# Optimization experiments

Hardware: AMD Instinct MI355X
Metric: run time of the kernel (lower is better)

The kernel has to match this reference:

```python
import jax, jax.numpy as jnp
import numpy as np

T, B, E, H, L = 512, 64, 300, 800, 3  # seq, batch, embed, per-layer hidden, layers


def setup_inputs() -> dict:
    key = jax.random.key(0)
    ks = jax.random.split(key, 8)
    s = 0.05
    return {
        "sent": jax.random.normal(ks[0], (T, B, E), jnp.float32),
        "lengths": jax.random.randint(ks[1], (B,), 1, T + 1),
        "W0": jax.random.normal(ks[2], (E, 3 * H), jnp.float32) * s,
        "b0": jnp.zeros((3 * H,), jnp.float32),
        "W1": jax.random.normal(ks[3], (H, 3 * H), jnp.float32) * s,
        "b1": jnp.zeros((3 * H,), jnp.float32),
        "W2": jax.random.normal(ks[4], (H, 3 * H), jnp.float32) * s,
        "b2": jnp.zeros((3 * H,), jnp.float32),
    }


def _fo_pool(f, z):
    # c_t = f_t * z_t + (1 - f_t) * c_{t-1}, c_0 = 0  (ForgetMult)
    # linear recurrence c_t = a_t * c_{t-1} + b_t with a = 1-f, b = f*z
    a = 1.0 - f
    b = f * z
    def comb(c1, c2):
        a1, b1 = c1
        a2, b2 = c2
        return (a2 * a1, a2 * b1 + b2)
    _, C = jax.lax.associative_scan(comb, (a, b), axis=0)
    return C  # [T,B,H]; initial state is zero so C is exactly the pooled state


def _qrnn_layer(x, W, b):
    g = jnp.einsum('tbe,eh->tbh', x, W) + b  # [T,B,3H]
    z, f, o = jnp.split(g, 3, axis=-1)
    C = _fo_pool(jax.nn.sigmoid(f), jnp.tanh(z))
    return jax.nn.sigmoid(o) * C, C[-1]


def reference(sent, lengths, W0, b0, W1, b1, W2, b2):
    h = sent
    finals = []
    for W, bb in ((W0, b0), (W1, b1), (W2, b2)):
        h, c_last = _qrnn_layer(h, W, bb)
        finals.append(c_last)
    hn = jnp.stack(finals, axis=0)            # [L,B,H]
    out = jnp.transpose(hn, (1, 0, 2)).reshape(B, L * H)  # [B, L*H]
    return out
```

## Files before the change

### kernel.cpp

```cpp
#include <hip/hip_runtime.h>
#include <hip/hip_bf16.h>
#include <cstdint>
#include <cstddef>


typedef __bf16 bf16_t;
typedef __bf16 bf16x8 __attribute__((ext_vector_type(8)));
typedef float f32x4 __attribute__((ext_vector_type(4)));

#define T_C 128
#define NCHUNK 4
#define BATCH 64
#define EMB 300
#define HID 800
#define LDH 832
#define MC (T_C * BATCH)
#define CAST_OPS (MC * 320 / 8)

__device__ __forceinline__ float fast_sigmoid(float x) {
  return 1.0f / (1.0f + __expf(-x));
}
__device__ __forceinline__ float fast_tanh(float x) {
  return 2.0f / (1.0f + __expf(-2.0f * x)) - 1.0f;
}
__device__ __forceinline__ float b2f(uint32_t u) {
  union { uint32_t i; float f; } x;
  x.i = u << 16;
  return x.f;
}

__device__ __forceinline__ void cast_op(const float* __restrict__ X,
                                        bf16_t* __restrict__ Y, int cc,
                                        int id) {
  const int rr = id / 40, cb = id - rr * 40;
  const int b = rr >> 7, t = rr & 127;
  const float* src = X + (size_t)((cc * 128 + t) * 64 + b) * EMB + cb * 8;
  bf16x8 w;
  if (cb < 37) {
    const f32x4 v0 = *(const f32x4*)src;
    const f32x4 v1 = *(const f32x4*)(src + 4);
#pragma unroll
    for (int e = 0; e < 4; ++e) {
      w[e] = (bf16_t)v0[e];
      w[e + 4] = (bf16_t)v1[e];
    }
  } else {
#pragma unroll
    for (int e = 0; e < 8; ++e) {
      const int col = cb * 8 + e;
      w[e] = (bf16_t)((col < EMB) ? src[e] : 0.0f);
    }
  }
  *(bf16x8*)&Y[((size_t)cc * MC + rr) * 320 + cb * 8] = w;
}

__global__ __launch_bounds__(256) void prep_all(
    const float* __restrict__ W0, const float* __restrict__ W1,
    const float* __restrict__ W2, bf16_t* __restrict__ M0,
    bf16_t* __restrict__ M1, bf16_t* __restrict__ Z2,
    const float* __restrict__ sent, bf16_t* __restrict__ A0) {
  const int z = blockIdx.z;
  if (z == 3) {
    const int id = (blockIdx.y * gridDim.x + blockIdx.x) * 256 + threadIdx.x;
    if (id < CAST_OPS) cast_op(sent, A0, 0, id);
    return;
  }
  const float* W = z == 0 ? W0 : (z == 1 ? W1 : W2);
  bf16_t* Wt = z == 0 ? M0 : (z == 1 ? M1 : Z2);
  const int K = z == 0 ? 300 : 800;
  const int Kpad = z == 0 ? 320 : 832;
  const int Npad = (z < 2) ? 2496 : 1664;
  const int i = blockIdx.x, j = blockIdx.y;
  if (i * 32 >= Npad || j * 32 >= Kpad) return;
  __shared__ float tile[32][33];
  const int tx = threadIdx.x & 31, ty = threadIdx.x >> 5;
#pragma unroll
  for (int r = 0; r < 32; r += 8) {
    const int k = j * 32 + ty + r;
    const int n = i * 32 + tx;
    int h, src;
    if (z < 2) {
      const int jt = n / 192, rr = n - jt * 192;
      if (rr < 128) {
        h = jt * 64 + (rr >> 1);
        src = (rr & 1) * 800 + h;
      } else {
        h = jt * 64 + (rr - 128);
        src = 1600 + h;
      }
    } else {
      h = n >> 1;
      src = (n & 1) * 800 + h;
    }
    const bool valid = (k < K) && (h < 800);
    tile[ty + r][tx] = valid ? W[(size_t)k * 2400 + src] : 0.0f;
  }
  __syncthreads();
#pragma unroll
  for (int r = 0; r < 32; r += 8) {
    const int n = i * 32 + ty + r, k = j * 32 + tx;
    if (n < Npad && k < Kpad)
      Wt[(size_t)n * Kpad + k] = (bf16_t)tile[tx][ty + r];
  }
}

__device__ __forceinline__ void stage16(const bf16_t* gp, bf16_t* lp) {
  __builtin_amdgcn_global_load_lds((__attribute__((address_space(1))) void*)gp,
                                   (__attribute__((address_space(3))) void*)lp,
                                   16, 0, 0);
}

template <int NTF, int ETS>
__device__ __forceinline__ void gemm_tile_to_lds(
    const bf16_t* __restrict__ A, const bf16_t* __restrict__ Bt,
    bf16_t* __restrict__ S, int K, int mBase, int nBase) {
  bf16_t* As = S;
  bf16_t* Bs = S + 8192;
  const int tid = threadIdx.x;
  const int wave = tid >> 6, lane = tid & 63;
  const int wm = wave >> 1, wn = wave & 1;
  const int srow = tid >> 3;
  const int scolSw = ((tid & 7) ^ (srow & 7)) * 8;
  const size_t aBase = (size_t)(mBase + srow) * K + scolSw;
  const size_t bBase = (size_t)(nBase + srow) * K + scolSw;
  const int ldsOff = tid * 8;

  f32x4 acc[4][NTF];
#pragma unroll
  for (int mt = 0; mt < 4; ++mt)
#pragma unroll
    for (int nt = 0; nt < NTF; ++nt) {
      f32x4 zz = {0.0f, 0.0f, 0.0f, 0.0f};
      acc[mt][nt] = zz;
    }

  const int fr = lane & 15, fq = lane >> 4;
  const int x0 = fr & 7;
  const int ckEl0 = (fq ^ x0) * 8;
  const int ckEl1 = ((4 + fq) ^ x0) * 8;

  for (int k0 = 0; k0 < K; k0 += 64) {
#pragma unroll
    for (int p = 0; p < 4; ++p)
      stage16(A + aBase + (size_t)(32 * p) * K + k0, &As[ldsOff + p * 2048]);
#pragma unroll
    for (int p = 0; p < NTF; ++p)
      stage16(Bt + bBase + (size_t)(32 * p) * K + k0, &Bs[ldsOff + p * 2048]);
    __syncthreads();
#pragma unroll
    for (int kh = 0; kh < 2; ++kh) {
      const int ck = kh ? ckEl1 : ckEl0;
      bf16x8 af[4], bfv[NTF];
#pragma unroll
      for (int mt = 0; mt < 4; ++mt)
        af[mt] = *(const bf16x8*)&As[(wm * 64 + mt * 16 + fr) * 64 + ck];
#pragma unroll
      for (int nt = 0; nt < NTF; ++nt)
        bfv[nt] = *(const bf16x8*)&Bs[(wn * (16 * NTF) + nt * 16 + fr) * 64 + ck];
#pragma unroll
      for (int mt = 0; mt < 4; ++mt)
#pragma unroll
        for (int nt = 0; nt < NTF; ++nt)
          acc[mt][nt] = __builtin_amdgcn_mfma_f32_16x16x32_bf16(
              af[mt], bfv[nt], acc[mt][nt], 0, 0, 0);
    }
    __syncthreads();
  }
  bf16_t* Et = S;
#pragma unroll
  for (int mt = 0; mt < 4; ++mt)
#pragma unroll
    for (int nt = 0; nt < NTF; ++nt)
#pragma unroll
      for (int r = 0; r < 4; ++r)
        Et[(wm * 64 + mt * 16 + fq * 4 + r) * ETS + wn * (16 * NTF) + nt * 16 +
           fr] = (bf16_t)acc[mt][nt][r];
  __syncthreads();
}

__device__ __forceinline__ void scan_h_body(
    const bf16_t* __restrict__ A, const bf16_t* __restrict__ Wm,
    const float* __restrict__ bias, bf16_t* __restrict__ Hout,
    float* __restrict__ carry, float* __restrict__ outC, int K, int outOff,
    int first, int last, int b, int ntile, bf16_t* S, float (*SA)[64],
    float (*SB)[64], float (*SC)[64]) {
  gemm_tile_to_lds<6, 196>(A, Wm, S, K, b * 128, ntile * 192);

  const uint32_t* Ep = (const uint32_t*)S;
  const int tid = threadIdx.x;
  const int hl = tid & 63, s = tid >> 6;
  const int h = ntile * 64 + hl;
  const bool hOK = (h < HID);
  const int hb = hOK ? h : 0;
  const float bz = bias[hb], bf = bias[hb + 800], bo = bias[hb + 1600];

  float av[32], bv[32];
  float Aa = 1.0f, Bb = 0.0f;
#pragma unroll
  for (int q = 0; q < 32; ++q) {
    const int t = s * 32 + q;
    const uint32_t v = Ep[t * 98 + hl];
    const float zv = fast_tanh(b2f(v & 0xffffu) + bz);
    const float fv = fast_sigmoid(b2f(v >> 16) + bf);
    av[q] = 1.0f - fv;
    bv[q] = fv * zv;
    Aa *= av[q];
    Bb = fmaf(av[q], Bb, bv[q]);
  }
  SA[s][hl] = Aa;
  SB[s][hl] = Bb;
  __syncthreads();
  if (tid < 64) {
    const int h2 = ntile * 64 + tid;
    const bool ok2 = (h2 < HID);
    float c = (first || !ok2) ? 0.0f : carry[b * HID + h2];
#pragma unroll
    for (int ss = 0; ss < 4; ++ss) {
      SC[ss][tid] = c;
      c = fmaf(SA[ss][tid], c, SB[ss][tid]);
    }
    if (ok2) {
      carry[b * HID + h2] = c;
      if (last) outC[b * 2400 + outOff + h2] = c;
    }
  }
  __syncthreads();
  float c = SC[s][hl];
#pragma unroll
  for (int q = 0; q < 32; ++q) {
    const int t = s * 32 + q;
    c = fmaf(av[q], c, bv[q]);
    const float o = fast_sigmoid((float)S[t * 196 + 128 + hl] + bo);
    Hout[(size_t)(b * 128 + t) * LDH + h] =
        hOK ? (bf16_t)(o * c) : (bf16_t)0.0f;
  }
}

__device__ __forceinline__ void scan_c_body(
    const bf16_t* __restrict__ A, const bf16_t* __restrict__ Wzf,
    const float* __restrict__ bias, float* __restrict__ carry,
    float* __restrict__ outC, int K, int outOff, int first, int last, int b,
    int ntile, bf16_t* S, float (*SA)[64], float (*SB)[64]) {
  gemm_tile_to_lds<4, 140>(A, Wzf, S, K, b * 128, ntile * 128);

  const uint32_t* Ep = (const uint32_t*)S;
  const int tid = threadIdx.x;
  const int hl = tid & 63, s = tid >> 6;
  const int h = ntile * 64 + hl;
  const int hb = (h < HID) ? h : 0;
  const float bz = bias[hb], bf = bias[hb + 800];

  float Aa = 1.0f, Bb = 0.0f;
#pragma unroll
  for (int q = 0; q < 32; ++q) {
    const int t = s * 32 + q;
    const uint32_t v = Ep[t * 70 + hl];
    const float zv = fast_tanh(b2f(v & 0xffffu) + bz);
    const float fv = fast_sigmoid(b2f(v >> 16) + bf);
    const float a = 1.0f - fv;
    Aa *= a;
    Bb = fmaf(a, Bb, fv * zv);
  }
  SA[s][hl] = Aa;
  SB[s][hl] = Bb;
  __syncthreads();
  if (tid < 64) {
    const int h2 = ntile * 64 + tid;
    const bool ok2 = (h2 < HID);
    float c = (first || !ok2) ? 0.0f : carry[b * HID + h2];
#pragma unroll
    for (int ss = 0; ss < 4; ++ss) c = fmaf(SA[ss][tid], c, SB[ss][tid]);
    if (ok2) {
      carry[b * HID + h2] = c;
      if (last) outC[b * 2400 + outOff + h2] = c;
    }
  }
}

__device__ __forceinline__ void block_tile(int& b, int& ntile) {
  const int nT = 13;
  const int L = blockIdx.y * nT + blockIdx.x;
  const int xcd = L & 7, j = L >> 3;
  b = xcd * 8 + j / nT;
  ntile = j % nT;
}

struct Role {
  const bf16_t* A;
  const bf16_t* W;
  const float* bias;
  bf16_t* Hout;
  float* carry;
  int K;
  int outOff;
  int type;
  int first;
  int last;
};

__global__ __launch_bounds__(256, 3) void gemm_scan_multi(
    Role r0, Role r1, Role r2, Role r3, float* __restrict__ outC) {
  __shared__ __align__(16) bf16_t S[25088];
  __shared__ float SA[4][64], SB[4][64], SC[4][64];
  const Role r = blockIdx.z == 0
                     ? r0
                     : (blockIdx.z == 1 ? r1 : (blockIdx.z == 2 ? r2 : r3));
  if (r.type == 3) {
    int id = (blockIdx.y * gridDim.x + blockIdx.x) * 256 + threadIdx.x;
    const int stride = gridDim.x * gridDim.y * 256;
#pragma unroll
    for (int it = 0; it < 2; ++it, id += stride)
      if (id < CAST_OPS) cast_op((const float*)r.A, r.Hout, r.outOff, id);
    return;
  }
  int b, ntile;
  block_tile(b, ntile);
  if (r.type == 1)
    scan_h_body(r.A, r.W, r.bias, r.Hout, r.carry, outC, r.K, r.outOff,
                r.first, r.last, b, ntile, S, SA, SB, SC);
  else
    scan_c_body(r.A, r.W, r.bias, r.carry, outC, r.K, r.outOff, r.first,
                r.last, b, ntile, S, SA, SB);
}

extern "C" void kernel_launch(void* const* d_in, const int* in_sizes, int n_in,
                              void* d_out, int out_size, void* d_ws, size_t ws_size,
                              hipStream_t stream) {
  const float* sent = (const float*)d_in[0];
  const float* W0 = (const float*)d_in[2];
  const float* b0 = (const float*)d_in[3];
  const float* W1 = (const float*)d_in[4];
  const float* b1 = (const float*)d_in[5];
  const float* W2 = (const float*)d_in[6];
  const float* b2 = (const float*)d_in[7];
  float* out = (float*)d_out;

  char* ws = (char*)d_ws;
  size_t off = 0;
  auto alloc = [&](size_t bytes) {
    void* p = ws + off;
    off += (bytes + 255) & ~(size_t)255;
    return p;
  };
  bf16_t* Wm0 = (bf16_t*)alloc((size_t)2496 * 320 * 2);
  bf16_t* Wm1 = (bf16_t*)alloc((size_t)2496 * 832 * 2);
  bf16_t* Wzf2 = (bf16_t*)alloc((size_t)1664 * 832 * 2);
  bf16_t* A0 = (bf16_t*)alloc((size_t)32768 * 320 * 2);
  bf16_t* H0buf[2], *H1buf[2];
  H0buf[0] = (bf16_t*)alloc((size_t)MC * LDH * 2);
  H0buf[1] = (bf16_t*)alloc((size_t)MC * LDH * 2);
  H1buf[0] = (bf16_t*)alloc((size_t)MC * LDH * 2);
  H1buf[1] = (bf16_t*)alloc((size_t)MC * LDH * 2);
  float* car0 = (float*)alloc((size_t)BATCH * HID * 4);
  float* car1 = (float*)alloc((size_t)BATCH * HID * 4);
  float* car2 = (float*)alloc((size_t)BATCH * HID * 4);
  if (off > ws_size) return;

  prep_all<<<dim3(78, 26, 4), 256, 0, stream>>>(W0, W1, W2, Wm0, Wm1, Wzf2,
                                                sent, A0);

  auto mkL0 = [&](int c) -> Role {
    return Role{A0 + (size_t)c * MC * 320, Wm0, b0, H0buf[c & 1], car0,
                320, 0, 1, c == 0, c == NCHUNK - 1};
  };
  auto mkL1 = [&](int c) -> Role {
    return Role{H0buf[c & 1], Wm1, b1, H1buf[c & 1], car1,
                832, 800, 1, c == 0, c == NCHUNK - 1};
  };
  auto mkL2 = [&](int c) -> Role {
    return Role{H1buf[c & 1], Wzf2, b2, nullptr, car2,
                832, 1600, 2, c == 0, c == NCHUNK - 1};
  };
  auto mkCast = [&](int c) -> Role {
    return Role{(const bf16_t*)sent, nullptr, nullptr, A0, nullptr,
                0, c, 3, 0, 0};
  };

  {
    Role a = mkL0(0), c1 = mkCast(1), c2 = mkCast(2), c3 = mkCast(3);
    gemm_scan_multi<<<dim3(13, 64, 4), 256, 0, stream>>>(a, c1, c2, c3, out);
  }
  {
    Role a = mkL1(0), b_ = mkL0(1);
    gemm_scan_multi<<<dim3(13, 64, 2), 256, 0, stream>>>(a, b_, b_, b_, out);
  }
  for (int c = 1; c <= 2; ++c) {
    Role a = mkL1(c), b_ = mkL2(c - 1), d = mkL0(c + 1);
    gemm_scan_multi<<<dim3(13, 64, 3), 256, 0, stream>>>(a, b_, d, d, out);
  }
  {
    Role a = mkL1(3), b_ = mkL2(2);
    gemm_scan_multi<<<dim3(13, 64, 2), 256, 0, stream>>>(a, b_, b_, b_, out);
  }
  {
    Role a = mkL2(3);
    gemm_scan_multi<<<dim3(13, 64, 1), 256, 0, stream>>>(a, a, a, a, out);
  }
}
```

Baseline: 465.4 us.

## Fold biases into GEMM via ones column; add dedicated last-chunk layer-2 kernel

Bias vectors are written into the padding row k==K of the transposed weight matrices. A matching constant 1.0 is placed in the first padding column of the activation inputs (the cast input and the hidden outputs at h==800), so the GEMM adds the bias itself and the epilogue no longer loads or adds it. A separate smaller-LDS kernel with launch bounds allowing 4 blocks per CU handles the final layer-2 chunk, replacing the generic multi-role kernel there. The bias is now rounded to bf16, which adds a little error, and the change relies on the padding columns being exactly 1 and 0.

```diff
diff --git a/kernel.cpp b/kernel.cpp
--- a/kernel.cpp
+++ b/kernel.cpp
@@ -48,7 +48,8 @@
 #pragma unroll
     for (int e = 0; e < 8; ++e) {
       const int col = cb * 8 + e;
-      w[e] = (bf16_t)((col < EMB) ? src[e] : 0.0f);
+      float v = (col < EMB) ? src[e] : (col == EMB ? 1.0f : 0.0f);
+      w[e] = (bf16_t)v;
     }
   }
   *(bf16x8*)&Y[((size_t)cc * MC + rr) * 320 + cb * 8] = w;
@@ -56,8 +57,9 @@
 
 __global__ __launch_bounds__(256) void prep_all(
     const float* __restrict__ W0, const float* __restrict__ W1,
-    const float* __restrict__ W2, bf16_t* __restrict__ M0,
-    bf16_t* __restrict__ M1, bf16_t* __restrict__ Z2,
+    const float* __restrict__ W2, const float* __restrict__ B0,
+    const float* __restrict__ B1, const float* __restrict__ B2,
+    bf16_t* __restrict__ M0, bf16_t* __restrict__ M1, bf16_t* __restrict__ Z2,
     const float* __restrict__ sent, bf16_t* __restrict__ A0) {
   const int z = blockIdx.z;
   if (z == 3) {
@@ -66,6 +68,7 @@
     return;
   }
   const float* W = z == 0 ? W0 : (z == 1 ? W1 : W2);
+  const float* Bv = z == 0 ? B0 : (z == 1 ? B1 : B2);
   bf16_t* Wt = z == 0 ? M0 : (z == 1 ? M1 : Z2);
   const int K = z == 0 ? 300 : 800;
   const int Kpad = z == 0 ? 320 : 832;
@@ -92,8 +95,12 @@
       h = n >> 1;
       src = (n & 1) * 800 + h;
     }
-    const bool valid = (k < K) && (h < 800);
-    tile[ty + r][tx] = valid ? W[(size_t)k * 2400 + src] : 0.0f;
+    float v = 0.0f;
+    if (h < 800) {
+      if (k < K) v = W[(size_t)k * 2400 + src];
+      else if (k == K) v = Bv[src];
+    }
+    tile[ty + r][tx] = v;
   }
   __syncthreads();
 #pragma unroll
@@ -180,10 +187,9 @@
 
 __device__ __forceinline__ void scan_h_body(
     const bf16_t* __restrict__ A, const bf16_t* __restrict__ Wm,
-    const float* __restrict__ bias, bf16_t* __restrict__ Hout,
-    float* __restrict__ carry, float* __restrict__ outC, int K, int outOff,
-    int first, int last, int b, int ntile, bf16_t* S, float (*SA)[64],
-    float (*SB)[64], float (*SC)[64]) {
+    bf16_t* __restrict__ Hout, float* __restrict__ carry,
+    float* __restrict__ outC, int K, int outOff, int first, int last, int b,
+    int ntile, bf16_t* S, float (*SA)[64], float (*SB)[64], float (*SC)[64]) {
   gemm_tile_to_lds<6, 196>(A, Wm, S, K, b * 128, ntile * 192);
 
   const uint32_t* Ep = (const uint32_t*)S;
@@ -191,8 +197,6 @@
   const int hl = tid & 63, s = tid >> 6;
   const int h = ntile * 64 + hl;
   const bool hOK = (h < HID);
-  const int hb = hOK ? h : 0;
-  const float bz = bias[hb], bf = bias[hb + 800], bo = bias[hb + 1600];
 
   float av[32], bv[32];
   float Aa = 1.0f, Bb = 0.0f;
@@ -200,8 +204,8 @@
   for (int q = 0; q < 32; ++q) {
     const int t = s * 32 + q;
     const uint32_t v = Ep[t * 98 + hl];
-    const float zv = fast_tanh(b2f(v & 0xffffu) + bz);
-    const float fv = fast_sigmoid(b2f(v >> 16) + bf);
+    const float zv = fast_tanh(b2f(v & 0xffffu));
+    const float fv = fast_sigmoid(b2f(v >> 16));
     av[q] = 1.0f - fv;
     bv[q] = fv * zv;
     Aa *= av[q];
@@ -225,38 +229,35 @@
     }
   }
   __syncthreads();
+  const bf16_t padv = (h == HID) ? (bf16_t)1.0f : (bf16_t)0.0f;
   float c = SC[s][hl];
 #pragma unroll
   for (int q = 0; q < 32; ++q) {
     const int t = s * 32 + q;
     c = fmaf(av[q], c, bv[q]);
-    const float o = fast_sigmoid((float)S[t * 196 + 128 + hl] + bo);
-    Hout[(size_t)(b * 128 + t) * LDH + h] =
-        hOK ? (bf16_t)(o * c) : (bf16_t)0.0f;
+    const float o = fast_sigmoid((float)S[t * 196 + 128 + hl]);
+    Hout[(size_t)(b * 128 + t) * LDH + h] = hOK ? (bf16_t)(o * c) : padv;
   }
 }
 
 __device__ __forceinline__ void scan_c_body(
     const bf16_t* __restrict__ A, const bf16_t* __restrict__ Wzf,
-    const float* __restrict__ bias, float* __restrict__ carry,
-    float* __restrict__ outC, int K, int outOff, int first, int last, int b,
-    int ntile, bf16_t* S, float (*SA)[64], float (*SB)[64]) {
+    float* __restrict__ carry, float* __restrict__ outC, int K, int outOff,
+    int first, int last, int b, int ntile, bf16_t* S, float (*SA)[64],
+    float (*SB)[64]) {
   gemm_tile_to_lds<4, 140>(A, Wzf, S, K, b * 128, ntile * 128);
 
   const uint32_t* Ep = (const uint32_t*)S;
   const int tid = threadIdx.x;
   const int hl = tid & 63, s = tid >> 6;
-  const int h = ntile * 64 + hl;
-  const int hb = (h < HID) ? h : 0;
-  const float bz = bias[hb], bf = bias[hb + 800];
 
   float Aa = 1.0f, Bb = 0.0f;
 #pragma unroll
   for (int q = 0; q < 32; ++q) {
     const int t = s * 32 + q;
     const uint32_t v = Ep[t * 70 + hl];
-    const float zv = fast_tanh(b2f(v & 0xffffu) + bz);
-    const float fv = fast_sigmoid(b2f(v >> 16) + bf);
+    const float zv = fast_tanh(b2f(v & 0xffffu));
+    const float fv = fast_sigmoid(b2f(v >> 16));
     const float a = 1.0f - fv;
     Aa *= a;
     Bb = fmaf(a, Bb, fv * zv);
@@ -288,7 +289,6 @@
 struct Role {
   const bf16_t* A;
   const bf16_t* W;
-  const float* bias;
   bf16_t* Hout;
   float* carry;
   int K;
@@ -316,11 +316,23 @@
   int b, ntile;
   block_tile(b, ntile);
   if (r.type == 1)
-    scan_h_body(r.A, r.W, r.bias, r.Hout, r.carry, outC, r.K, r.outOff,
-                r.first, r.last, b, ntile, S, SA, SB, SC);
+    scan_h_body(r.A, r.W, r.Hout, r.carry, outC, r.K, r.outOff, r.first,
+                r.last, b, ntile, S, SA, SB, SC);
   else
-    scan_c_body(r.A, r.W, r.bias, r.carry, outC, r.K, r.outOff, r.first,
-                r.last, b, ntile, S, SA, SB);
+    scan_c_body(r.A, r.W, r.carry, outC, r.K, r.outOff, r.first, r.last, b,
+                ntile, S, SA, SB);
+}
+
+__global__ __launch_bounds__(256, 4) void gemm_scan_c4(
+    const bf16_t* __restrict__ A, const bf16_t* __restrict__ Wzf,
+    float* __restrict__ carry, float* __restrict__ outC, int K, int outOff,
+    int first, int last) {
+  __shared__ __align__(16) bf16_t S[17920];
+  __shared__ float SA[4][64], SB[4][64];
+  int b, ntile;
+  block_tile(b, ntile);
+  scan_c_body(A, Wzf, carry, outC, K, outOff, first, last, b, ntile, S, SA,
+              SB);
 }
 
 extern "C" void kernel_launch(void* const* d_in, const int* in_sizes, int n_in,
@@ -356,24 +368,23 @@
   float* car2 = (float*)alloc((size_t)BATCH * HID * 4);
   if (off > ws_size) return;
 
-  prep_all<<<dim3(78, 26, 4), 256, 0, stream>>>(W0, W1, W2, Wm0, Wm1, Wzf2,
-                                                sent, A0);
+  prep_all<<<dim3(78, 26, 4), 256, 0, stream>>>(W0, W1, W2, b0, b1, b2, Wm0,
+                                                Wm1, Wzf2, sent, A0);
 
   auto mkL0 = [&](int c) -> Role {
-    return Role{A0 + (size_t)c * MC * 320, Wm0, b0, H0buf[c & 1], car0,
+    return Role{A0 + (size_t)c * MC * 320, Wm0, H0buf[c & 1], car0,
                 320, 0, 1, c == 0, c == NCHUNK - 1};
   };
   auto mkL1 = [&](int c) -> Role {
-    return Role{H0buf[c & 1], Wm1, b1, H1buf[c & 1], car1,
+    return Role{H0buf[c & 1], Wm1, H1buf[c & 1], car1,
                 832, 800, 1, c == 0, c == NCHUNK - 1};
   };
   auto mkL2 = [&](int c) -> Role {
-    return Role{H1buf[c & 1], Wzf2, b2, nullptr, car2,
+    return Role{H1buf[c & 1], Wzf2, nullptr, car2,
                 832, 1600, 2, c == 0, c == NCHUNK - 1};
   };
   auto mkCast = [&](int c) -> Role {
-    return Role{(const bf16_t*)sent, nullptr, nullptr, A0, nullptr,
-                0, c, 3, 0, 0};
+    return Role{(const bf16_t*)sent, nullptr, A0, nullptr, 0, c, 3, 0, 0};
   };
 
   {
@@ -392,8 +403,6 @@
     Role a = mkL1(3), b_ = mkL2(2);
     gemm_scan_multi<<<dim3(13, 64, 2), 256, 0, stream>>>(a, b_, b_, b_, out);
   }
-  {
-    Role a = mkL2(3);
-    gemm_scan_multi<<<dim3(13, 64, 1), 256, 0, stream>>>(a, a, a, a, out);
-  }
-}
+  gemm_scan_c4<<<dim3(13, 64), 256, 0, stream>>>(H1buf[1], Wzf2, car2, out,
+                                                 832, 1600, 0, 1);
+}
```

Result: no change. 461.7 us (-0.8%).
